# Optimization experiments

Hardware: AMD Instinct MI355X
Metric: run time of the kernel (lower is better)

Reference implementation:

```python
import jax, jax.numpy as jnp
import numpy as np

NEG_INF = -1e30


def setup_inputs() -> dict:
    key = jax.random.key(0)
    kx, km, kq, kk, kv, ko = jax.random.split(key, 6)
    B, D, L = 2, 1024, 2048
    H, DK = 16, 64
    x = jax.random.normal(kx, (B, D, L), dtype=jnp.float32)
    mask = (jax.random.uniform(km, (B, L)) < 0.9).astype(jnp.float32)
    # per-head projection weights, stacked: (H, D, DK); output proj (D, H*DK)==(D, D)
    sq = 1.0 / np.sqrt(D)
    Wq = jax.random.normal(kq, (H, D, DK), dtype=jnp.float32) * sq
    Wk = jax.random.normal(kk, (H, D, DK), dtype=jnp.float32) * sq
    Wv = jax.random.normal(kv, (H, D, DK), dtype=jnp.float32) * sq
    Wo = jax.random.normal(ko, (D, H * DK), dtype=jnp.float32) * sq
    return {"x": x, "mask": mask, "Wq": Wq, "Wk": Wk, "Wv": Wv, "Wo": Wo}


def reference(x, mask, Wq, Wk, Wv, Wo):
    # x: (B, D, L); original transposes to (B, L, D)
    B, D, L = x.shape
    H, _, DK = Wq.shape
    xt = jnp.transpose(x, (0, 2, 1))  # (B, L, D)
    q = jnp.einsum('bld,hdk->bhlk', xt, Wq)
    k = jnp.einsum('bld,hdk->bhlk', xt, Wk)
    v = jnp.einsum('bld,hdk->bhlk', xt, Wv)
    scores = jnp.einsum('bhlk,bhmk->bhlm', q, k) * (1.0 / np.sqrt(DK))
    # masked log-softmax over keys (hmask), squad-style: mask*logit + (1-mask)*-1e30
    hmask = mask[:, None, None, :]  # (B,1,1,Lk)
    masked = hmask * scores + (1.0 - hmask) * NEG_INF
    logp = jax.nn.log_softmax(masked, axis=-1)
    # second softmax over the log-probs, then multiplicative vmask on query dim
    p = jax.nn.softmax(logp, axis=-1) * mask[:, None, :, None]
    heads = jnp.einsum('bhlm,bhmk->bhlk', p, v)  # (B,H,L,DK)
    head = jnp.transpose(heads, (0, 2, 1, 3)).reshape(B, L, H * DK)
    out = jnp.einsum('ble,de->bld', head, Wo)  # matmul(head, Wo) with Wo (D, H*DK)... 
    # NOTE: torch.matmul(head, Wo) treats Wo as (H*DK_in, D_out) only if square; here
    # Wo is (D, H*DK) with D == H*DK, and torch contracts head's last dim with Wo's FIRST dim:
    out = head @ Wo  # (B, L, H*DK) @ (D, H*DK) requires D==H*DK; contracts dim 0 of Wo
    return jnp.transpose(out, (0, 2, 1))  # (B, D, L)


if __name__ == "__main__":
    print(reference(**setup_inputs()).shape)
```

## Files before the change

kernel.cpp:

```cpp
#include <hip/hip_runtime.h>
#include <hip/hip_bf16.h>

typedef unsigned short u16;
typedef unsigned int u32;
typedef unsigned long long u64;
typedef short s8v __attribute__((ext_vector_type(8)));
typedef short s4v __attribute__((ext_vector_type(4)));
typedef __bf16 bfv8 __attribute__((ext_vector_type(8)));
typedef float f4 __attribute__((ext_vector_type(4)));

static constexpr int B = 2, D = 1024, L = 2048, H = 16, DK = 64, E = 1024;
static constexpr float QSCALE = 0.125f * 1.44269504088896340736f;
static constexpr float SMB = -16.0f;
static constexpr float MASKB = -12000.0f;

#define DEV __device__ __forceinline__

DEV u16 f2bf(float f) {
  unsigned int u = __float_as_uint(f);
  u += 0x7FFFu + ((u >> 16) & 1u);
  return (u16)(u >> 16);
}
DEV float fexp2(float x) { return __builtin_amdgcn_exp2f(x); }
DEV u32 pkbf(float a, float b) {
  __hip_bfloat162 h = __float22bfloat162_rn(float2{a, b});
  u32 r;
  __builtin_memcpy(&r, &h, 4);
  return r;
}
DEV bfv8 cat8(s4v a, s4v b) {
  s8v r;
#pragma unroll
  for (int i = 0; i < 4; ++i) {
    r[i] = a[i];
    r[i + 4] = b[i];
  }
  return __builtin_bit_cast(bfv8, r);
}
DEV int kperm(int kk) {
  return (kk & 96) | (((kk >> 2) & 3) << 3) | (((kk >> 4) & 1) << 2) |
         (kk & 3);
}

#define GLD_LDS16(gp, lp)                                                     \
  __builtin_amdgcn_global_load_lds(                                           \
      (const __attribute__((address_space(1))) void*)(gp),                    \
      (__attribute__((address_space(3))) void*)(lp), 16, 0, 0)

__global__ __launch_bounds__(256) void k_prep(
    const float* __restrict__ x, const float* __restrict__ Wq,
    const float* __restrict__ Wk, const float* __restrict__ Wv,
    const float* __restrict__ Wo, u16* __restrict__ xt, u16* __restrict__ Wt,
    u16* __restrict__ WoT) {
  __shared__ u16 t[64][67];
  const int tid = threadIdx.x;
  const int g = blockIdx.x;
  const float* src;
  u16* dst;
  int sld, dld;
  if (g < 1024) {
    const int b = g >> 9, dt = (g >> 5) & 15, lt = g & 31;
    src = x + ((size_t)b * D + dt * 64) * L + lt * 64;
    sld = L;
    dst = xt + ((size_t)b * L + lt * 64) * D + dt * 64;
    dld = D;
  } else if (g < 1792) {
    const int u = g - 1024;
    const int w = u >> 8, h = (u >> 4) & 15, dt = u & 15;
    const float* Ws = (w == 0) ? Wq : ((w == 1) ? Wk : Wv);
    src = Ws + ((size_t)h * D + dt * 64) * DK;
    sld = DK;
    dst = Wt + ((size_t)(w * H + h) * DK) * D + dt * 64;
    dld = D;
  } else {
    const int v = g - 1792;
    const int et = v >> 4, dt = v & 15;
    src = Wo + ((size_t)et * 64) * D + dt * 64;
    sld = D;
    dst = WoT + ((size_t)dt * 64) * E + et * 64;
    dld = E;
  }
  const int r = tid >> 2, c16 = (tid & 3) * 16;
#pragma unroll
  for (int j = 0; j < 16; j += 4) {
    const f4 v4 = *(const f4*)(src + (size_t)r * sld + c16 + j);
    t[r][c16 + j]     = f2bf(v4[0]);
    t[r][c16 + j + 1] = f2bf(v4[1]);
    t[r][c16 + j + 2] = f2bf(v4[2]);
    t[r][c16 + j + 3] = f2bf(v4[3]);
  }
  __syncthreads();
  s8v o0, o1;
#pragma unroll
  for (int i = 0; i < 8; ++i) {
    o0[i] = (short)t[c16 + i][r];
    o1[i] = (short)t[c16 + 8 + i][r];
  }
  *(s8v*)(dst + (size_t)r * dld + c16)     = o0;
  *(s8v*)(dst + (size_t)r * dld + c16 + 8) = o1;
}

template <int AR, int BR>
DEV void gemm_tile(const u16* __restrict__ A, const u16* __restrict__ Bt,
                   int arow0, int brow0, u16* As, u16* Bs,
                   f4 (&acc)[AR / 32][BR / 32]) {
  const int tid = threadIdx.x;
  const int wid = tid >> 6, lane = tid & 63;
  const int q = lane >> 4, ln = lane & 15;
  const int wr = wid >> 1, wc = wid & 1;
  const int lrow = lane >> 3;
  const int lc = (lane & 7) ^ lrow;
  const int f0 = (q ^ (ln & 7)) * 8;
  const int f1 = ((q + 4) ^ (ln & 7)) * 8;
  constexpr int MT = AR / 32, NT = BR / 32;

  for (int k0 = 0; k0 < 1024; k0 += 64) {
    __syncthreads();
#pragma unroll
    for (int j = 0; j < AR / 32; ++j) {
      const int rb = wid * (AR / 4) + j * 8;
      GLD_LDS16(A + (size_t)(arow0 + rb + lrow) * 1024 + k0 + lc * 8,
                As + rb * 64);
    }
#pragma unroll
    for (int j = 0; j < BR / 32; ++j) {
      const int rb = wid * (BR / 4) + j * 8;
      GLD_LDS16(Bt + (size_t)(brow0 + rb + lrow) * 1024 + k0 + lc * 8,
                Bs + rb * 64);
    }
    __syncthreads();
#pragma unroll
    for (int ks = 0; ks < 2; ++ks) {
      const int fc = ks ? f1 : f0;
      bfv8 af[MT], bf[NT];
#pragma unroll
      for (int mt = 0; mt < MT; ++mt)
        af[mt] = *(const bfv8*)(As + (wr * (AR / 2) + mt * 16 + ln) * 64 + fc);
#pragma unroll
      for (int nt = 0; nt < NT; ++nt)
        bf[nt] = *(const bfv8*)(Bs + (wc * (BR / 2) + nt * 16 + ln) * 64 + fc);
#pragma unroll
      for (int mt = 0; mt < MT; ++mt)
#pragma unroll
        for (int nt = 0; nt < NT; ++nt)
          acc[mt][nt] = __builtin_amdgcn_mfma_f32_16x16x32_bf16(
              af[mt], bf[nt], acc[mt][nt], 0, 0, 0);
    }
  }
}

__global__ __launch_bounds__(256, 3) void k_qkvg(
    const u16* __restrict__ xt, const u16* __restrict__ Wt,
    u16* __restrict__ Q, u16* __restrict__ K, u16* __restrict__ Vt) {
  __shared__ u16 As[128 * 64];
  __shared__ u16 Bs[128 * 64];
  const int orig = blockIdx.x;
  const int xcd = orig & 7, kk = orig >> 3;
  const int bm = (xcd >> 1) * 8 + (kk & 7);
  const int bn = (xcd & 1) * 12 + (kk >> 3);
  f4 acc[4][4];
#pragma unroll
  for (int mt = 0; mt < 4; ++mt)
#pragma unroll
    for (int nt = 0; nt < 4; ++nt) acc[mt][nt] = (f4){0.f, 0.f, 0.f, 0.f};
  gemm_tile<128, 128>(xt, Wt, bm * 128, bn * 128, As, Bs, acc);

  const int tid = threadIdx.x, wid = tid >> 6, lane = tid & 63;
  const int q = lane >> 4, ln = lane & 15;
  const int wr = wid >> 1, wc = wid & 1;
  const int h2 = bn * 2 + wc;
  const int wsel = h2 >> 4, h = h2 & 15;
  const int b = bm >> 4;
  const int lbase = (bm & 15) * 128 + wr * 64;
  if (wsel == 0) {
    u16* dst = Q + (size_t)(b * H + h) * L * DK;
#pragma unroll
    for (int mt = 0; mt < 4; ++mt)
#pragma unroll
      for (int nt = 0; nt < 4; ++nt)
#pragma unroll
        for (int r = 0; r < 4; ++r)
          dst[(size_t)(lbase + mt * 16 + q * 4 + r) * DK + nt * 16 + ln] =
              f2bf(acc[mt][nt][r] * QSCALE);
  } else if (wsel == 1) {
    u16* dst = K + (size_t)(b * H + h) * L * DK;
#pragma unroll
    for (int mt = 0; mt < 4; ++mt)
#pragma unroll
      for (int nt = 0; nt < 4; ++nt)
#pragma unroll
        for (int r = 0; r < 4; ++r)
          dst[(size_t)(lbase + mt * 16 + q * 4 + r) * DK + nt * 16 + ln] =
              f2bf(acc[mt][nt][r]);
  } else {
    u16* dst = Vt + (size_t)(b * H + h) * DK * L;
#pragma unroll
    for (int mt = 0; mt < 4; ++mt)
#pragma unroll
      for (int nt = 0; nt < 4; ++nt) {
        const u64 pk = (u64)pkbf(acc[mt][nt][0], acc[mt][nt][1]) |
                       ((u64)pkbf(acc[mt][nt][2], acc[mt][nt][3]) << 32);
        *(u64*)(dst + (size_t)(nt * 16 + ln) * L + lbase + mt * 16 + q * 4) =
            pk;
      }
  }
}

__global__ __launch_bounds__(512, 4) void k_attn(
    const u16* __restrict__ Q, const u16* __restrict__ K,
    const u16* __restrict__ Vt, const float* __restrict__ mask,
    u16* __restrict__ Hd) {
  __shared__ __align__(16) u16 smem[20480];
  u16* kt = smem;
  u16* vt = smem + 8192;
  float* mb = (float*)(smem + 16384);
  const int orig = blockIdx.x;
  const int xcd = orig & 7, kk2 = orig >> 3;
  const int bh = xcd * 4 + (kk2 >> 4);
  const int lt = kk2 & 15;
  const int b = bh >> 4, h = bh & 15;
  const int tid = threadIdx.x;
  const int w = tid >> 6, lane = tid & 63, q = lane >> 4, ln = lane & 15;
  const int wq = w >> 1, wk = w & 1;
  for (int i = tid; i < L; i += 512)
    mb[i] = (mask[(size_t)b * L + i] != 0.0f) ? SMB : MASKB;

  const u16* Qp = Q + (size_t)bh * L * DK;
  const u16* Kp = K + (size_t)bh * L * DK;
  const u16* Vp = Vt + (size_t)bh * DK * L;
  const int lq = lt * 128 + wq * 32;

  bfv8 qf[2][2];
#pragma unroll
  for (int mt = 0; mt < 2; ++mt) {
    qf[mt][0] = *(const bfv8*)(Qp + (size_t)(lq + mt * 16 + ln) * DK + q * 8);
    qf[mt][1] =
        *(const bfv8*)(Qp + (size_t)(lq + mt * 16 + ln) * DK + 32 + q * 8);
  }

  const int lrow = lane >> 3;
  const int lc = (lane & 7) ^ lrow;
  const int c0 = (q ^ (ln & 7)) * 8;
  const int c1 = ((q + 4) ^ (ln & 7)) * 8;
  int kpr[2];
#pragma unroll
  for (int j = 0; j < 2; ++j) kpr[j] = kperm(w * 16 + j * 8 + lrow);

  auto stage = [&](int m0) {
#pragma unroll
    for (int j = 0; j < 2; ++j) {
      GLD_LDS16(Kp + (size_t)(m0 + kpr[j]) * DK + lc * 8,
                kt + (w * 16 + j * 8) * 64);
    }
    const int fr = w * 8 + lrow;
#pragma unroll
    for (int kh = 0; kh < 2; ++kh) {
      GLD_LDS16(Vp + (size_t)fr * L + m0 + kh * 64 + lc * 8,
                vt + kh * 4096 + (w * 8) * 64);
    }
  };

  union {
    f4 v;
    float f[4];
  } ot[2][4];
#pragma unroll
  for (int mt = 0; mt < 2; ++mt)
#pragma unroll
    for (int dt = 0; dt < 4; ++dt) ot[mt][dt].v = (f4){0.f, 0.f, 0.f, 0.f};
  float lp[2] = {0.f, 0.f};

  for (int it = 0; it < L / 128; ++it) {
    const int m0 = it * 128;
    __syncthreads();
    stage(m0);
    __syncthreads();
    const u16* ktc = kt;
    const u16* vtc = vt + (wk >> 0) * 0 + (wk) * 0 + ((wk) ? 0 : 0);
    vtc = vt + ((wk * 64) >> 6) * 4096;

    s4v pbe[2];
    bfv8 pbx[2][2];
#pragma unroll
    for (int nt = 0; nt < 4; ++nt) {
      const int krow = wk * 64 + nt * 16 + ln;
      const bfv8 kf0 = *(const bfv8*)(ktc + krow * 64 + c0);
      const bfv8 kf1 = *(const bfv8*)(ktc + krow * 64 + c1);
      const f4 mbv = *(const f4*)(mb + m0 + wk * 64 + (nt >> 1) * 32 +
                                  (nt & 1) * 4 + q * 8);
#pragma unroll
      for (int mt = 0; mt < 2; ++mt) {
        f4 a = mbv;
        __builtin_amdgcn_s_setprio(1);
        a = __builtin_amdgcn_mfma_f32_16x16x32_bf16(kf0, qf[mt][0], a, 0, 0,
                                                    0);
        a = __builtin_amdgcn_mfma_f32_16x16x32_bf16(kf1, qf[mt][1], a, 0, 0,
                                                    0);
        __builtin_amdgcn_s_setprio(0);
        const float p0 = fexp2(a[0]);
        const float p1 = fexp2(a[1]);
        const float p2 = fexp2(a[2]);
        const float p3 = fexp2(a[3]);
        lp[mt] += (p0 + p1) + (p2 + p3);
        const u64 pk = (u64)pkbf(p0, p1) | ((u64)pkbf(p2, p3) << 32);
        const s4v pc = __builtin_bit_cast(s4v, pk);
        if (nt & 1)
          pbx[mt][nt >> 1] = cat8(pbe[mt], pc);
        else
          pbe[mt] = pc;
      }
    }
    __builtin_amdgcn_s_setprio(1);
#pragma unroll
    for (int g = 0; g < 2; ++g) {
#pragma unroll
      for (int dt = 0; dt < 4; ++dt) {
        const int vrow = dt * 16 + ln;
        const bfv8 av =
            *(const bfv8*)(vtc + vrow * 64 + (((g * 4 + q) ^ (ln & 7)) * 8));
#pragma unroll
        for (int mt = 0; mt < 2; ++mt)
          ot[mt][dt].v = __builtin_amdgcn_mfma_f32_16x16x32_bf16(
              av, pbx[mt][g], ot[mt][dt].v, 0, 0, 0);
      }
    }
    __builtin_amdgcn_s_setprio(0);
  }
#pragma unroll
  for (int mt = 0; mt < 2; ++mt) {
    lp[mt] += __shfl_xor(lp[mt], 16);
    lp[mt] += __shfl_xor(lp[mt], 32);
  }
  float* sOt = (float*)smem;
  float* sLp = (float*)(smem + 16384);
  __syncthreads();
  if (wk) {
#pragma unroll
    for (int mt = 0; mt < 2; ++mt) {
#pragma unroll
      for (int dt = 0; dt < 4; ++dt)
        *(f4*)(sOt + ((((wq * 2 + mt) * 4 + dt) * 64) + lane) * 4) =
            ot[mt][dt].v;
      sLp[(wq * 2 + mt) * 64 + lane] = lp[mt];
    }
  }
  __syncthreads();
  if (!wk) {
#pragma unroll
    for (int mt = 0; mt < 2; ++mt) {
#pragma unroll
      for (int dt = 0; dt < 4; ++dt)
        ot[mt][dt].v +=
            *(const f4*)(sOt + ((((wq * 2 + mt) * 4 + dt) * 64) + lane) * 4);
      lp[mt] += sLp[(wq * 2 + mt) * 64 + lane];
      const float mv = mask[(size_t)b * L + lq + mt * 16 + ln];
      const float linv = (mv != 0.0f) ? (1.0f / lp[mt]) : 0.0f;
#pragma unroll
      for (int dt = 0; dt < 4; ++dt) {
        const u64 pk =
            (u64)pkbf(ot[mt][dt].f[0] * linv, ot[mt][dt].f[1] * linv) |
            ((u64)pkbf(ot[mt][dt].f[2] * linv, ot[mt][dt].f[3] * linv) << 32);
        *(u64*)(Hd + (size_t)(b * L + lq + mt * 16 + ln) * E + h * DK +
                dt * 16 + q * 4) = pk;
      }
    }
  }
}

__global__ __launch_bounds__(256, 4) void k_projg(const u16* __restrict__ WoT,
                                                  const u16* __restrict__ Hd,
                                                  float* __restrict__ out) {
  __shared__ u16 As[64 * 64];
  __shared__ u16 Bs[64 * 64];
  const int orig = blockIdx.x;
  const int xcd = orig & 7, kk = orig >> 3;
  const int bm = kk & 15;
  const int bn = xcd * 8 + (kk >> 4);
  f4 acc[2][2];
#pragma unroll
  for (int mt = 0; mt < 2; ++mt)
#pragma unroll
    for (int nt = 0; nt < 2; ++nt) acc[mt][nt] = (f4){0.f, 0.f, 0.f, 0.f};
  gemm_tile<64, 64>(WoT, Hd, bm * 64, bn * 64, As, Bs, acc);

  const int tid = threadIdx.x, wid = tid >> 6, lane = tid & 63;
  const int q = lane >> 4, ln = lane & 15;
  const int wr = wid >> 1, wc = wid & 1;
#pragma unroll
  for (int mt = 0; mt < 2; ++mt)
#pragma unroll
    for (int nt = 0; nt < 2; ++nt)
#pragma unroll
      for (int r = 0; r < 4; ++r) {
        const int d = bm * 64 + wr * 32 + mt * 16 + q * 4 + r;
        const int n = bn * 64 + wc * 32 + nt * 16 + ln;
        const int bb = n >> 11, l = n & 2047;
        out[((size_t)(bb * D + d)) * L + l] = acc[mt][nt][r];
      }
}

extern "C" void kernel_launch(void* const* d_in, const int* in_sizes, int n_in,
                              void* d_out, int out_size, void* d_ws,
                              size_t ws_size, hipStream_t stream) {
  const float* x    = (const float*)d_in[0];
  const float* mask = (const float*)d_in[1];
  const float* Wq   = (const float*)d_in[2];
  const float* Wk   = (const float*)d_in[3];
  const float* Wv   = (const float*)d_in[4];
  const float* Wo   = (const float*)d_in[5];
  u16* ws = (u16*)d_ws;
  u16* Qws  = ws;
  u16* Kws  = ws + 4194304;
  u16* Vtws = ws + 8388608;
  u16* WoTw = ws + 12582912;
  u16* Wtws = ws + 13631488;
  u16* xtws = ws + 16777216;
  u16* Hdws = ws + 16777216;

  k_prep<<<2048, 256, 0, stream>>>(x, Wq, Wk, Wv, Wo, xtws, Wtws, WoTw);
  k_qkvg<<<768, 256, 0, stream>>>(xtws, Wtws, Qws, Kws, Vtws);
  k_attn<<<512, 512, 0, stream>>>(Qws, Kws, Vtws, mask, Hdws);
  k_projg<<<1024, 256, 0, stream>>>(WoTw, Hdws, (float*)d_out);
}
```

Baseline: 168.7 us.

## Split attention key tile across four waves and halve query tile per block

The attention kernel now gives each block 64 query rows instead of 128 and splits every 128-key tile across four waves of 32 keys each instead of two of 64. The grid doubles to 1024 blocks and the launch bound asks for higher occupancy. Partial outputs and row sums are combined through a two-stage shared-memory reduction. The aim is more parallelism and better latency hiding, at the cost of staging each K/V tile twice as often overall and extra reduction syncs.

```diff
diff --git a/kernel.cpp b/kernel.cpp
--- a/kernel.cpp
+++ b/kernel.cpp
@@ -206,7 +206,7 @@
   }
 }
 
-__global__ __launch_bounds__(512, 4) void k_attn(
+__global__ __launch_bounds__(512, 8) void k_attn(
     const u16* __restrict__ Q, const u16* __restrict__ K,
     const u16* __restrict__ Vt, const float* __restrict__ mask,
     u16* __restrict__ Hd) {
@@ -216,19 +216,19 @@
   float* mb = (float*)(smem + 16384);
   const int orig = blockIdx.x;
   const int xcd = orig & 7, kk2 = orig >> 3;
-  const int bh = xcd * 4 + (kk2 >> 4);
-  const int lt = kk2 & 15;
+  const int bh = xcd * 4 + (kk2 >> 5);
+  const int lt = kk2 & 31;
   const int b = bh >> 4, h = bh & 15;
   const int tid = threadIdx.x;
   const int w = tid >> 6, lane = tid & 63, q = lane >> 4, ln = lane & 15;
-  const int wq = w >> 1, wk = w & 1;
+  const int wq = w >> 2, wk = w & 3;
   for (int i = tid; i < L; i += 512)
     mb[i] = (mask[(size_t)b * L + i] != 0.0f) ? SMB : MASKB;
 
   const u16* Qp = Q + (size_t)bh * L * DK;
   const u16* Kp = K + (size_t)bh * L * DK;
   const u16* Vp = Vt + (size_t)bh * DK * L;
-  const int lq = lt * 128 + wq * 32;
+  const int lq = lt * 64 + wq * 32;
 
   bfv8 qf[2][2];
 #pragma unroll
@@ -276,18 +276,16 @@
     stage(m0);
     __syncthreads();
     const u16* ktc = kt;
-    const u16* vtc = vt + (wk >> 0) * 0 + (wk) * 0 + ((wk) ? 0 : 0);
-    vtc = vt + ((wk * 64) >> 6) * 4096;
+    const u16* vtc = vt + (wk >> 1) * 4096;
 
     s4v pbe[2];
-    bfv8 pbx[2][2];
-#pragma unroll
-    for (int nt = 0; nt < 4; ++nt) {
-      const int krow = wk * 64 + nt * 16 + ln;
+    bfv8 pbx[2];
+#pragma unroll
+    for (int nt = 0; nt < 2; ++nt) {
+      const int krow = wk * 32 + nt * 16 + ln;
       const bfv8 kf0 = *(const bfv8*)(ktc + krow * 64 + c0);
       const bfv8 kf1 = *(const bfv8*)(ktc + krow * 64 + c1);
-      const f4 mbv = *(const f4*)(mb + m0 + wk * 64 + (nt >> 1) * 32 +
-                                  (nt & 1) * 4 + q * 8);
+      const f4 mbv = *(const f4*)(mb + m0 + wk * 32 + nt * 4 + q * 8);
 #pragma unroll
       for (int mt = 0; mt < 2; ++mt) {
         f4 a = mbv;
@@ -304,25 +302,22 @@
         lp[mt] += (p0 + p1) + (p2 + p3);
         const u64 pk = (u64)pkbf(p0, p1) | ((u64)pkbf(p2, p3) << 32);
         const s4v pc = __builtin_bit_cast(s4v, pk);
-        if (nt & 1)
-          pbx[mt][nt >> 1] = cat8(pbe[mt], pc);
+        if (nt)
+          pbx[mt] = cat8(pbe[mt], pc);
         else
           pbe[mt] = pc;
       }
     }
+    const int cb = (((wk & 1) * 4 + q) ^ (ln & 7)) * 8;
     __builtin_amdgcn_s_setprio(1);
 #pragma unroll
-    for (int g = 0; g < 2; ++g) {
-#pragma unroll
-      for (int dt = 0; dt < 4; ++dt) {
-        const int vrow = dt * 16 + ln;
-        const bfv8 av =
-            *(const bfv8*)(vtc + vrow * 64 + (((g * 4 + q) ^ (ln & 7)) * 8));
-#pragma unroll
-        for (int mt = 0; mt < 2; ++mt)
-          ot[mt][dt].v = __builtin_amdgcn_mfma_f32_16x16x32_bf16(
-              av, pbx[mt][g], ot[mt][dt].v, 0, 0, 0);
-      }
+    for (int dt = 0; dt < 4; ++dt) {
+      const int vrow = dt * 16 + ln;
+      const bfv8 av = *(const bfv8*)(vtc + vrow * 64 + cb);
+#pragma unroll
+      for (int mt = 0; mt < 2; ++mt)
+        ot[mt][dt].v = __builtin_amdgcn_mfma_f32_16x16x32_bf16(
+            av, pbx[mt], ot[mt][dt].v, 0, 0, 0);
     }
     __builtin_amdgcn_s_setprio(0);
   }
@@ -331,28 +326,69 @@
     lp[mt] += __shfl_xor(lp[mt], 16);
     lp[mt] += __shfl_xor(lp[mt], 32);
   }
-  float* sOt = (float*)smem;
-  float* sLp = (float*)(smem + 16384);
+  float* sA = (float*)smem;
+  float* sB = (float*)(smem + 8192);
+  float* sL = (float*)(smem + 16384);
   __syncthreads();
-  if (wk) {
+  if (wk == 1) {
+#pragma unroll
+    for (int mt = 0; mt < 2; ++mt)
+#pragma unroll
+      for (int dt = 0; dt < 4; ++dt)
+        *(f4*)(sA + (((wq * 2 + mt) * 4 + dt) * 64 + lane) * 4) =
+            ot[mt][dt].v;
+  }
+  if (wk == 3) {
+#pragma unroll
+    for (int mt = 0; mt < 2; ++mt)
+#pragma unroll
+      for (int dt = 0; dt < 4; ++dt)
+        *(f4*)(sB + (((wq * 2 + mt) * 4 + dt) * 64 + lane) * 4) =
+            ot[mt][dt].v;
+  }
+  if (wk != 0 && q == 0) {
+#pragma unroll
+    for (int mt = 0; mt < 2; ++mt)
+      sL[(((wk - 1) * 2 + wq) * 2 + mt) * 16 + ln] = lp[mt];
+  }
+  __syncthreads();
+  if (wk == 0) {
 #pragma unroll
     for (int mt = 0; mt < 2; ++mt) {
 #pragma unroll
       for (int dt = 0; dt < 4; ++dt)
-        *(f4*)(sOt + ((((wq * 2 + mt) * 4 + dt) * 64) + lane) * 4) =
+        ot[mt][dt].v +=
+            *(const f4*)(sA + (((wq * 2 + mt) * 4 + dt) * 64 + lane) * 4);
+      lp[mt] += sL[((0 * 2 + wq) * 2 + mt) * 16 + ln] +
+                sL[((1 * 2 + wq) * 2 + mt) * 16 + ln] +
+                sL[((2 * 2 + wq) * 2 + mt) * 16 + ln];
+    }
+  }
+  if (wk == 2) {
+#pragma unroll
+    for (int mt = 0; mt < 2; ++mt)
+#pragma unroll
+      for (int dt = 0; dt < 4; ++dt)
+        ot[mt][dt].v +=
+            *(const f4*)(sB + (((wq * 2 + mt) * 4 + dt) * 64 + lane) * 4);
+  }
+  __syncthreads();
+  if (wk == 2) {
+#pragma unroll
+    for (int mt = 0; mt < 2; ++mt)
+#pragma unroll
+      for (int dt = 0; dt < 4; ++dt)
+        *(f4*)(sA + (((wq * 2 + mt) * 4 + dt) * 64 + lane) * 4) =
             ot[mt][dt].v;
-      sLp[(wq * 2 + mt) * 64 + lane] = lp[mt];
-    }
   }
   __syncthreads();
-  if (!wk) {
+  if (wk == 0) {
 #pragma unroll
     for (int mt = 0; mt < 2; ++mt) {
 #pragma unroll
       for (int dt = 0; dt < 4; ++dt)
         ot[mt][dt].v +=
-            *(const f4*)(sOt + ((((wq * 2 + mt) * 4 + dt) * 64) + lane) * 4);
-      lp[mt] += sLp[(wq * 2 + mt) * 64 + lane];
+            *(const f4*)(sA + (((wq * 2 + mt) * 4 + dt) * 64 + lane) * 4);
       const float mv = mask[(size_t)b * L + lq + mt * 16 + ln];
       const float linv = (mv != 0.0f) ? (1.0f / lp[mt]) : 0.0f;
 #pragma unroll
@@ -419,6 +455,6 @@
 
   k_prep<<<2048, 256, 0, stream>>>(x, Wq, Wk, Wv, Wo, xtws, Wtws, WoTw);
   k_qkvg<<<768, 256, 0, stream>>>(xtws, Wtws, Qws, Kws, Vtws);
-  k_attn<<<512, 512, 0, stream>>>(Qws, Kws, Vtws, mask, Hdws);
+  k_attn<<<1024, 512, 0, stream>>>(Qws, Kws, Vtws, mask, Hdws);
   k_projg<<<1024, 256, 0, stream>>>(WoTw, Hdws, (float*)d_out);
 }
```

Measured after the change: 468.1 us. 2.77x slower.
